# Performance work log

Measured on AMD Instinct MI355X. Metric: run time of the kernel, lower is better.

Reference implementation:

```python
import jax, jax.numpy as jnp
import numpy as np

NUM_CAPSULE = 16
DIM_CAPSULE = 32
ROUTINGS = 4
EPS = 1e-07


def squash(x, axis=-1):
    # NOTE: faithful to the source: x / sqrt(sum(x^2) + eps) (unit-norm style),
    # NOT the standard Hinton squash.
    s2 = jnp.sum(x * x, axis=axis, keepdims=True)
    return x / jnp.sqrt(s2 + EPS)


def setup_inputs() -> dict:
    key = jax.random.key(0)
    k1, k2 = jax.random.split(key)
    B, N_in, D_in = 128, 1024, 256
    x = jax.random.normal(k1, (B, N_in, D_in), dtype=jnp.float32)
    # xavier_normal over (1, D_in, NUM_CAPSULE*DIM_CAPSULE)
    fan_in, fan_out = D_in, NUM_CAPSULE * DIM_CAPSULE
    std = np.sqrt(2.0 / (fan_in + fan_out))
    W = jax.random.normal(k2, (1, D_in, NUM_CAPSULE * DIM_CAPSULE), dtype=jnp.float32) * std
    return {"x": x, "W": W}


def reference(x, W):
    B, N_in, _ = x.shape
    # u_hat: [B, N_in, num_cap*dim_cap] -> [B, num_cap, N_in, dim_cap]
    u_hat = jnp.matmul(x, W[0])
    u_hat = u_hat.reshape(B, N_in, NUM_CAPSULE, DIM_CAPSULE).transpose(0, 2, 1, 3)

    b = jnp.zeros((B, NUM_CAPSULE, N_in), dtype=u_hat.dtype)
    outputs = None
    for i in range(ROUTINGS):
        # torch permutes to softmax over the num_capsule axis; equivalent to axis=1 here
        c = jax.nn.softmax(b, axis=1)                      # [B, num_cap, N_in]
        outputs = squash(jnp.einsum('bij,bijk->bik', c, u_hat))  # [B, num_cap, dim_cap]
        if i < ROUTINGS - 1:
            b = jnp.einsum('bik,bijk->bij', outputs, u_hat)
    return outputs
```

## Files before the change

kernel.cpp:

```cpp
#include <hip/hip_runtime.h>

typedef unsigned int u32;
typedef unsigned short u16;
typedef float f32x4 __attribute__((ext_vector_type(4)));
typedef __bf16 bf16x8 __attribute__((ext_vector_type(8)));

#define BATCH 128
#define NIN   1024
#define DIN   256
#define NC    16
#define DC    32
#define NCOL  512

__device__ __forceinline__ float bflo(u32 v){ return __uint_as_float(v << 16); }
__device__ __forceinline__ float bfhi(u32 v){ return __uint_as_float(v & 0xffff0000u); }
__device__ __forceinline__ u32 bfround(u32 ua){ return (ua + 0x7fffu + ((ua >> 16) & 1u)) >> 16; }
__device__ __forceinline__ u32 pack2(float a, float b){
    return (bfround(__float_as_uint(a)) & 0xffffu) | (bfround(__float_as_uint(b)) << 16);
}
__device__ __forceinline__ bf16x8 ldfrag(const u16* p){
    return __builtin_bit_cast(bf16x8, *(const uint4*)p);
}

__device__ __forceinline__ int lds_x(int r, int d){
    int sw = (d >> 2) ^ ((r & 7) << 1) ^ (((r >> 3) & 3) << 2);
    return r * 256 + (sw << 2) + (d & 3);
}

__global__ __launch_bounds__(256) void k_pre(const float* __restrict__ x, const float* __restrict__ W,
                                             uint4* __restrict__ xbT, u16* __restrict__ xb,
                                             float* __restrict__ s, uint2* __restrict__ Wb,
                                             uint2* __restrict__ WT){
    __shared__ __align__(16) u16 xt[64 * 256];
    const int t = threadIdx.x, jc8 = blockIdx.x, b = blockIdx.y;

    if (jc8 == 0){
        int id = b * 256 + t;
        float4 w4 = ((const float4*)W)[id];
        Wb[id] = make_uint2(pack2(w4.x, w4.y), pack2(w4.z, w4.w));
        int c = id >> 6, d4 = id & 63;
        float e0 = W[(size_t)(d4 * 4 + 0) * NCOL + c];
        float e1 = W[(size_t)(d4 * 4 + 1) * NCOL + c];
        float e2 = W[(size_t)(d4 * 4 + 2) * NCOL + c];
        float e3 = W[(size_t)(d4 * 4 + 3) * NCOL + c];
        WT[c * 64 + d4] = make_uint2(pack2(e0, e1), pack2(e2, e3));
    }
    {
        const float4* xg = (const float4*)(x + ((size_t)b * NIN + jc8 * 64) * DIN);
        uint2* xbw = (uint2*)xb + ((size_t)(b * NIN + jc8 * 64)) * 64;
        int d4 = t & 63;
        #pragma unroll
        for (int m = 0; m < 16; m++){
            int r = (t >> 6) + 4 * m;
            float4 v = xg[r * 64 + d4];
            uint2 p = make_uint2(pack2(v.x, v.y), pack2(v.z, v.w));
            *(uint2*)&xt[lds_x(r, d4 * 4)] = p;
            xbw[r * 64 + d4] = p;
        }
    }
    __syncthreads();
    {
        float acc = 0.f;
        #pragma unroll
        for (int r = 0; r < 64; r++) acc += bflo((u32)xt[lds_x(r, t)]);
        atomicAdd(&s[b * DIN + t], acc);
    }
    #pragma unroll
    for (int w = 0; w < 8; w++){
        int oid = t + 256 * w;
        int lane = oid & 63, js2 = (oid >> 6) & 1, dt = oid >> 7;
        int l15 = lane & 15, q = lane >> 4;
        int rb = js2 * 32 + q * 8, d = dt * 16 + l15;
        u32 r[4];
        #pragma unroll
        for (int p = 0; p < 4; p++){
            u32 lo = xt[lds_x(rb + 2 * p, d)];
            u32 hi = xt[lds_x(rb + 2 * p + 1, d)];
            r[p] = lo | (hi << 16);
        }
        xbT[(((size_t)b * 16 + dt) * 32 + (jc8 * 2 + js2)) * 64 + lane] = make_uint4(r[0], r[1], r[2], r[3]);
    }
}

__global__ __launch_bounds__(256) void k_main(const u16* __restrict__ xb, const uint4* __restrict__ xbT,
                                              const u16* __restrict__ vb, float* __restrict__ zp){
    __shared__ float bbl[16][132];
    __shared__ __align__(16) u16 cl[16][136];
    const int t = threadIdx.x, jh = blockIdx.x, b = blockIdx.y;
    const int lane = t & 63, wv = t >> 6;
    const int l15 = lane & 15, q = lane >> 4;

    uint4 vfrag[8];
    #pragma unroll
    for (int ks = 0; ks < 8; ks++)
        vfrag[ks] = *(const uint4*)&vb[((size_t)b * 16 + l15) * 256 + ks * 32 + q * 8];

    const u16* xrow = xb + ((size_t)(b * NIN + jh * 128)) * 256;
    #pragma unroll
    for (int u = 0; u < 2; u++){
        int jt = wv * 2 + u;
        const u16* xr = xrow + (jt * 16 + l15) * 256 + q * 8;
        f32x4 acc = {0.f, 0.f, 0.f, 0.f};
        #pragma unroll
        for (int ks = 0; ks < 8; ks++)
            acc = __builtin_amdgcn_mfma_f32_16x16x32_bf16(
                __builtin_bit_cast(bf16x8, vfrag[ks]), ldfrag(xr + ks * 32), acc, 0, 0, 0);
        #pragma unroll
        for (int r = 0; r < 4; r++) bbl[q * 4 + r][jt * 16 + l15] = acc[r];
    }
    __syncthreads();

    if (t < 128){
        float mx = -1e30f, e[16], sum = 0.f;
        #pragma unroll
        for (int i = 0; i < 16; i++) mx = fmaxf(mx, bbl[i][t]);
        #pragma unroll
        for (int i = 0; i < 16; i++){ e[i] = __expf(bbl[i][t] - mx); sum += e[i]; }
        float inv = 1.f / sum;
        #pragma unroll
        for (int i = 0; i < 16; i++) cl[i][t] = (u16)bfround(__float_as_uint(e[i] * inv));
    }
    __syncthreads();

    bf16x8 cfrag[4];
    #pragma unroll
    for (int ksj = 0; ksj < 4; ksj++)
        cfrag[ksj] = __builtin_bit_cast(bf16x8, *(const uint4*)&cl[l15][ksj * 32 + q * 8]);
    #pragma unroll
    for (int u = 0; u < 4; u++){
        int dt = wv * 4 + u;
        f32x4 acc = {0.f, 0.f, 0.f, 0.f};
        #pragma unroll
        for (int ksj = 0; ksj < 4; ksj++){
            uint4 bw = xbT[(((size_t)b * 16 + dt) * 32 + jh * 4 + ksj) * 64 + lane];
            acc = __builtin_amdgcn_mfma_f32_16x16x32_bf16(
                cfrag[ksj], __builtin_bit_cast(bf16x8, bw), acc, 0, 0, 0);
        }
        float* zpb = zp + ((((size_t)jh * 128 + b) * 16) * 256) + dt * 16 + l15;
        #pragma unroll
        for (int r = 0; r < 4; r++) zpb[(size_t)(q * 4 + r) * 256] = acc[r];
    }
}

__global__ __launch_bounds__(256) void k_tail(const float* __restrict__ s, const float* __restrict__ zp,
                                              const u16* __restrict__ Wb, const u32* __restrict__ WT32,
                                              u16* __restrict__ vb, float* __restrict__ out, int mode){
    __shared__ float zl[8][260];
    __shared__ __align__(16) float ol[256];
    const int ih2 = blockIdx.x, b = blockIdx.y, t = threadIdx.x;
    const int i_loc = t >> 5;
    const int o_idx = ih2 * 256 + t;
    float y = 0.f;
    if (mode == 0){
        zl[0][t] = s[b * 256 + t] * (1.f / 16.f);
        __syncthreads();
        #pragma unroll 8
        for (int d = 0; d < 256; d++) y += zl[0][d] * bflo((u32)Wb[d * 512 + o_idx]);
    } else {
        #pragma unroll
        for (int u0 = 0; u0 < 8; u0++){
            int idx = t + 256 * u0;
            int ii = idx >> 8, dd = idx & 255;
            int ig = ih2 * 8 + ii;
            float acc = 0.f;
            #pragma unroll
            for (int jh = 0; jh < 8; jh++)
                acc += zp[((((size_t)jh * 128 + b) * 16 + ig) * 256) + dd];
            zl[ii][dd] = acc;
        }
        __syncthreads();
        #pragma unroll 8
        for (int d = 0; d < 256; d++) y += zl[i_loc][d] * bflo((u32)Wb[d * 512 + o_idx]);
    }
    float s2 = y * y;
    s2 += __shfl_xor(s2, 1); s2 += __shfl_xor(s2, 2); s2 += __shfl_xor(s2, 4);
    s2 += __shfl_xor(s2, 8); s2 += __shfl_xor(s2, 16);
    float r = y / sqrtf(s2 + 1e-7f);
    if (mode == 2){ out[b * 512 + o_idx] = r; return; }
    ol[t] = r;
    __syncthreads();
    {
        int dh = t & 127, ihalf = t >> 7;
        #pragma unroll
        for (int e = 0; e < 4; e++){
            int ii = ihalf * 4 + e;
            int i2 = ih2 * 8 + ii;
            float a0 = 0.f, a1 = 0.f;
            #pragma unroll
            for (int k = 0; k < 32; k++){
                u32 wv2 = WT32[(size_t)(i2 * 32 + k) * 128 + dh];
                float ok = ol[ii * 32 + k];
                a0 += ok * bflo(wv2); a1 += ok * bfhi(wv2);
            }
            ((u32*)vb)[(size_t)(b * 16 + i2) * 128 + dh] = pack2(a0, a1);
        }
    }
}

extern "C" void kernel_launch(void* const* d_in, const int* in_sizes, int n_in,
                              void* d_out, int out_size, void* d_ws, size_t ws_size,
                              hipStream_t stream){
    const float* x = (const float*)d_in[0];
    const float* W = (const float*)d_in[1];
    float* out = (float*)d_out;
    char* ws = (char*)d_ws;
    float* s    = (float*)(ws);
    u16*   vb   = (u16*)  (ws + 131072);
    u16*   Wb   = (u16*)  (ws + 1179648);
    u32*   WT   = (u32*)  (ws + 1441792);
    float* zp   = (float*)(ws + 1703936);
    u16*   xb   = (u16*)  (ws + 18481152);
    uint4* xbT  = (uint4*)(ws + 85590016);

    hipMemsetAsync(s, 0, 131072, stream);
    k_pre<<<dim3(16, BATCH), 256, 0, stream>>>(x, W, xbT, xb, s, (uint2*)Wb, (uint2*)WT);
    k_tail<<<dim3(2, BATCH), 256, 0, stream>>>(s, zp, Wb, WT, vb, out, 0);
    for (int it = 1; it < 4; it++){
        k_main<<<dim3(8, BATCH), 256, 0, stream>>>(xb, xbT, vb, zp);
        k_tail<<<dim3(2, BATCH), 256, 0, stream>>>(s, zp, Wb, WT, vb, out, it == 3 ? 2 : 1);
    }
}
```

Measured before the change: 361.9 us.

## Fuse routing iterations into one per-batch kernel and shrink preprocessing tiles

Replaces the seven alternating k_main/k_tail launches with a single k_fused kernel that runs one 1024-thread block per batch. That block does all routing iterations in shared memory, so the zp partial-sum round trips through global memory and the extra launches go away. k_pre now uses 32-row tiles and computes column sums in registers during conversion instead of in a second LDS pass. The trade-off is that only 128 blocks run, which lowers parallelism, and the fused block uses a lot of shared memory, which limits occupancy.

```diff
diff --git a/kernel.cpp b/kernel.cpp
--- a/kernel.cpp
+++ b/kernel.cpp
@@ -31,10 +31,10 @@
                                              uint4* __restrict__ xbT, u16* __restrict__ xb,
                                              float* __restrict__ s, uint2* __restrict__ Wb,
                                              uint2* __restrict__ WT){
-    __shared__ __align__(16) u16 xt[64 * 256];
-    const int t = threadIdx.x, jc8 = blockIdx.x, b = blockIdx.y;
-
-    if (jc8 == 0){
+    __shared__ __align__(16) u16 xt[32 * 256];
+    const int t = threadIdx.x, jc = blockIdx.x, b = blockIdx.y;
+
+    if (jc == 0){
         int id = b * 256 + t;
         float4 w4 = ((const float4*)W)[id];
         Wb[id] = make_uint2(pack2(w4.x, w4.y), pack2(w4.z, w4.w));
@@ -46,31 +46,32 @@
         WT[c * 64 + d4] = make_uint2(pack2(e0, e1), pack2(e2, e3));
     }
     {
-        const float4* xg = (const float4*)(x + ((size_t)b * NIN + jc8 * 64) * DIN);
-        uint2* xbw = (uint2*)xb + ((size_t)(b * NIN + jc8 * 64)) * 64;
-        int d4 = t & 63;
+        const float4* xg = (const float4*)(x + ((size_t)b * NIN + jc * 32) * DIN);
+        uint2* xbw = (uint2*)xb + ((size_t)(b * NIN + jc * 32)) * 64;
+        int d4 = t & 63, rg = t >> 6;
+        float cs0 = 0.f, cs1 = 0.f, cs2 = 0.f, cs3 = 0.f;
         #pragma unroll
-        for (int m = 0; m < 16; m++){
-            int r = (t >> 6) + 4 * m;
+        for (int m = 0; m < 8; m++){
+            int r = rg + 4 * m;
             float4 v = xg[r * 64 + d4];
             uint2 p = make_uint2(pack2(v.x, v.y), pack2(v.z, v.w));
             *(uint2*)&xt[lds_x(r, d4 * 4)] = p;
             xbw[r * 64 + d4] = p;
-        }
+            cs0 += bflo(p.x); cs1 += bfhi(p.x);
+            cs2 += bflo(p.y); cs3 += bfhi(p.y);
+        }
+        atomicAdd(&s[b * DIN + d4 * 4 + 0], cs0);
+        atomicAdd(&s[b * DIN + d4 * 4 + 1], cs1);
+        atomicAdd(&s[b * DIN + d4 * 4 + 2], cs2);
+        atomicAdd(&s[b * DIN + d4 * 4 + 3], cs3);
     }
     __syncthreads();
-    {
-        float acc = 0.f;
-        #pragma unroll
-        for (int r = 0; r < 64; r++) acc += bflo((u32)xt[lds_x(r, t)]);
-        atomicAdd(&s[b * DIN + t], acc);
-    }
     #pragma unroll
-    for (int w = 0; w < 8; w++){
+    for (int w = 0; w < 4; w++){
         int oid = t + 256 * w;
-        int lane = oid & 63, js2 = (oid >> 6) & 1, dt = oid >> 7;
+        int lane = oid & 63, dt = oid >> 6;
         int l15 = lane & 15, q = lane >> 4;
-        int rb = js2 * 32 + q * 8, d = dt * 16 + l15;
+        int rb = q * 8, d = dt * 16 + l15;
         u32 r[4];
         #pragma unroll
         for (int p = 0; p < 4; p++){
@@ -78,121 +79,118 @@
             u32 hi = xt[lds_x(rb + 2 * p + 1, d)];
             r[p] = lo | (hi << 16);
         }
-        xbT[(((size_t)b * 16 + dt) * 32 + (jc8 * 2 + js2)) * 64 + lane] = make_uint4(r[0], r[1], r[2], r[3]);
-    }
-}
-
-__global__ __launch_bounds__(256) void k_main(const u16* __restrict__ xb, const uint4* __restrict__ xbT,
-                                              const u16* __restrict__ vb, float* __restrict__ zp){
-    __shared__ float bbl[16][132];
-    __shared__ __align__(16) u16 cl[16][136];
-    const int t = threadIdx.x, jh = blockIdx.x, b = blockIdx.y;
+        xbT[(((size_t)b * 16 + dt) * 32 + jc) * 64 + lane] = make_uint4(r[0], r[1], r[2], r[3]);
+    }
+}
+
+__global__ __launch_bounds__(1024) void k_fused(const u16* __restrict__ xb, const uint4* __restrict__ xbT,
+                                                const float* __restrict__ s, const u16* __restrict__ Wb,
+                                                const u32* __restrict__ WT32, float* __restrict__ out){
+    __shared__ float bbl[16 * 1028];
+    __shared__ __align__(16) u16 cl[16 * 1032];
+    __shared__ float zl[16 * 260];
+    __shared__ __align__(16) float ol[512];
+    __shared__ __align__(16) u32 vfb[8 * 256];
+    __shared__ float yp[1024];
+    const int b = blockIdx.x, t = threadIdx.x;
     const int lane = t & 63, wv = t >> 6;
     const int l15 = lane & 15, q = lane >> 4;
 
-    uint4 vfrag[8];
-    #pragma unroll
-    for (int ks = 0; ks < 8; ks++)
-        vfrag[ks] = *(const uint4*)&vb[((size_t)b * 16 + l15) * 256 + ks * 32 + q * 8];
-
-    const u16* xrow = xb + ((size_t)(b * NIN + jh * 128)) * 256;
-    #pragma unroll
-    for (int u = 0; u < 2; u++){
-        int jt = wv * 2 + u;
-        const u16* xr = xrow + (jt * 16 + l15) * 256 + q * 8;
-        f32x4 acc = {0.f, 0.f, 0.f, 0.f};
-        #pragma unroll
-        for (int ks = 0; ks < 8; ks++)
-            acc = __builtin_amdgcn_mfma_f32_16x16x32_bf16(
-                __builtin_bit_cast(bf16x8, vfrag[ks]), ldfrag(xr + ks * 32), acc, 0, 0, 0);
-        #pragma unroll
-        for (int r = 0; r < 4; r++) bbl[q * 4 + r][jt * 16 + l15] = acc[r];
-    }
-    __syncthreads();
-
-    if (t < 128){
-        float mx = -1e30f, e[16], sum = 0.f;
-        #pragma unroll
-        for (int i = 0; i < 16; i++) mx = fmaxf(mx, bbl[i][t]);
-        #pragma unroll
-        for (int i = 0; i < 16; i++){ e[i] = __expf(bbl[i][t] - mx); sum += e[i]; }
-        float inv = 1.f / sum;
-        #pragma unroll
-        for (int i = 0; i < 16; i++) cl[i][t] = (u16)bfround(__float_as_uint(e[i] * inv));
-    }
-    __syncthreads();
-
-    bf16x8 cfrag[4];
-    #pragma unroll
-    for (int ksj = 0; ksj < 4; ksj++)
-        cfrag[ksj] = __builtin_bit_cast(bf16x8, *(const uint4*)&cl[l15][ksj * 32 + q * 8]);
-    #pragma unroll
-    for (int u = 0; u < 4; u++){
-        int dt = wv * 4 + u;
-        f32x4 acc = {0.f, 0.f, 0.f, 0.f};
-        #pragma unroll
-        for (int ksj = 0; ksj < 4; ksj++){
-            uint4 bw = xbT[(((size_t)b * 16 + dt) * 32 + jh * 4 + ksj) * 64 + lane];
-            acc = __builtin_amdgcn_mfma_f32_16x16x32_bf16(
-                cfrag[ksj], __builtin_bit_cast(bf16x8, bw), acc, 0, 0, 0);
-        }
-        float* zpb = zp + ((((size_t)jh * 128 + b) * 16) * 256) + dt * 16 + l15;
-        #pragma unroll
-        for (int r = 0; r < 4; r++) zpb[(size_t)(q * 4 + r) * 256] = acc[r];
-    }
-}
-
-__global__ __launch_bounds__(256) void k_tail(const float* __restrict__ s, const float* __restrict__ zp,
-                                              const u16* __restrict__ Wb, const u32* __restrict__ WT32,
-                                              u16* __restrict__ vb, float* __restrict__ out, int mode){
-    __shared__ float zl[8][260];
-    __shared__ __align__(16) float ol[256];
-    const int ih2 = blockIdx.x, b = blockIdx.y, t = threadIdx.x;
-    const int i_loc = t >> 5;
-    const int o_idx = ih2 * 256 + t;
-    float y = 0.f;
-    if (mode == 0){
-        zl[0][t] = s[b * 256 + t] * (1.f / 16.f);
-        __syncthreads();
-        #pragma unroll 8
-        for (int d = 0; d < 256; d++) y += zl[0][d] * bflo((u32)Wb[d * 512 + o_idx]);
-    } else {
-        #pragma unroll
-        for (int u0 = 0; u0 < 8; u0++){
-            int idx = t + 256 * u0;
-            int ii = idx >> 8, dd = idx & 255;
-            int ig = ih2 * 8 + ii;
-            float acc = 0.f;
-            #pragma unroll
-            for (int jh = 0; jh < 8; jh++)
-                acc += zp[((((size_t)jh * 128 + b) * 16 + ig) * 256) + dd];
-            zl[ii][dd] = acc;
-        }
-        __syncthreads();
-        #pragma unroll 8
-        for (int d = 0; d < 256; d++) y += zl[i_loc][d] * bflo((u32)Wb[d * 512 + o_idx]);
-    }
-    float s2 = y * y;
-    s2 += __shfl_xor(s2, 1); s2 += __shfl_xor(s2, 2); s2 += __shfl_xor(s2, 4);
-    s2 += __shfl_xor(s2, 8); s2 += __shfl_xor(s2, 16);
-    float r = y / sqrtf(s2 + 1e-7f);
-    if (mode == 2){ out[b * 512 + o_idx] = r; return; }
-    ol[t] = r;
+    if (t < 256) zl[t] = s[b * 256 + t] * (1.f / 16.f);
     __syncthreads();
     {
-        int dh = t & 127, ihalf = t >> 7;
+        int h = t >> 9, c = t & 511;
+        const u16* wp = Wb + (size_t)(h * 128) * 512 + c;
+        float acc = 0.f;
+        #pragma unroll 8
+        for (int d = 0; d < 128; d++) acc += zl[h * 128 + d] * bflo((u32)wp[d * 512]);
+        yp[t] = acc;
+    }
+    __syncthreads();
+    if (t < 512){
+        float yv = yp[t] + yp[t + 512];
+        float s2 = yv * yv;
+        s2 += __shfl_xor(s2, 1); s2 += __shfl_xor(s2, 2); s2 += __shfl_xor(s2, 4);
+        s2 += __shfl_xor(s2, 8); s2 += __shfl_xor(s2, 16);
+        ol[t] = yv / sqrtf(s2 + 1e-7f);
+    }
+
+    for (int it = 1; it <= 3; ++it){
+        __syncthreads();
         #pragma unroll
-        for (int e = 0; e < 4; e++){
-            int ii = ihalf * 4 + e;
-            int i2 = ih2 * 8 + ii;
+        for (int e2 = 0; e2 < 2; e2++){
+            int wo = t + 1024 * e2;
+            int i = wo >> 7, dh = wo & 127;
             float a0 = 0.f, a1 = 0.f;
             #pragma unroll
             for (int k = 0; k < 32; k++){
-                u32 wv2 = WT32[(size_t)(i2 * 32 + k) * 128 + dh];
-                float ok = ol[ii * 32 + k];
+                u32 wv2 = WT32[(size_t)(i * 32 + k) * 128 + dh];
+                float ok = ol[i * 32 + k];
                 a0 += ok * bflo(wv2); a1 += ok * bfhi(wv2);
             }
-            ((u32*)vb)[(size_t)(b * 16 + i2) * 128 + dh] = pack2(a0, a1);
+            int ks = dh >> 4, qq = (dh >> 2) & 3, e = dh & 3;
+            vfb[ks * 256 + (qq * 16 + i) * 4 + e] = pack2(a0, a1);
+        }
+        __syncthreads();
+        {
+            uint4 vf[8];
+            #pragma unroll
+            for (int ks = 0; ks < 8; ks++) vf[ks] = *(const uint4*)&vfb[ks * 256 + lane * 4];
+            #pragma unroll
+            for (int u = 0; u < 4; u++){
+                int jt = wv * 4 + u;
+                const u16* xr = xb + ((size_t)(b * NIN + jt * 16 + l15)) * 256 + q * 8;
+                f32x4 acc = {0.f, 0.f, 0.f, 0.f};
+                #pragma unroll
+                for (int ks = 0; ks < 8; ks++)
+                    acc = __builtin_amdgcn_mfma_f32_16x16x32_bf16(
+                        __builtin_bit_cast(bf16x8, vf[ks]), ldfrag(xr + ks * 32), acc, 0, 0, 0);
+                #pragma unroll
+                for (int r = 0; r < 4; r++) bbl[(q * 4 + r) * 1028 + jt * 16 + l15] = acc[r];
+            }
+        }
+        __syncthreads();
+        {
+            float mx = -1e30f, e[16], sum = 0.f;
+            #pragma unroll
+            for (int i = 0; i < 16; i++) mx = fmaxf(mx, bbl[i * 1028 + t]);
+            #pragma unroll
+            for (int i = 0; i < 16; i++){ e[i] = __expf(bbl[i * 1028 + t] - mx); sum += e[i]; }
+            float inv = 1.f / sum;
+            #pragma unroll
+            for (int i = 0; i < 16; i++) cl[i * 1032 + t] = (u16)bfround(__float_as_uint(e[i] * inv));
+        }
+        __syncthreads();
+        {
+            int dt = wv;
+            f32x4 acc = {0.f, 0.f, 0.f, 0.f};
+            const uint4* xT = xbT + (((size_t)b * 16 + dt) * 32) * 64 + lane;
+            #pragma unroll 8
+            for (int js = 0; js < 32; js++){
+                bf16x8 cf = ldfrag(&cl[l15 * 1032 + js * 32 + q * 8]);
+                acc = __builtin_amdgcn_mfma_f32_16x16x32_bf16(cf, __builtin_bit_cast(bf16x8, xT[js * 64]), acc, 0, 0, 0);
+            }
+            #pragma unroll
+            for (int r = 0; r < 4; r++) zl[(q * 4 + r) * 260 + dt * 16 + l15] = acc[r];
+        }
+        __syncthreads();
+        {
+            int h = t >> 9, c = t & 511, i = c >> 5;
+            const u16* wp = Wb + (size_t)(h * 128) * 512 + c;
+            float acc = 0.f;
+            #pragma unroll 8
+            for (int d = 0; d < 128; d++) acc += zl[i * 260 + h * 128 + d] * bflo((u32)wp[d * 512]);
+            yp[t] = acc;
+        }
+        __syncthreads();
+        if (t < 512){
+            float yv = yp[t] + yp[t + 512];
+            float s2 = yv * yv;
+            s2 += __shfl_xor(s2, 1); s2 += __shfl_xor(s2, 2); s2 += __shfl_xor(s2, 4);
+            s2 += __shfl_xor(s2, 8); s2 += __shfl_xor(s2, 16);
+            float r = yv / sqrtf(s2 + 1e-7f);
+            if (it == 3) out[b * NCOL + t] = r;
+            else         ol[t] = r;
         }
     }
 }
@@ -205,18 +203,12 @@
     float* out = (float*)d_out;
     char* ws = (char*)d_ws;
     float* s    = (float*)(ws);
-    u16*   vb   = (u16*)  (ws + 131072);
-    u16*   Wb   = (u16*)  (ws + 1179648);
-    u32*   WT   = (u32*)  (ws + 1441792);
-    float* zp   = (float*)(ws + 1703936);
-    u16*   xb   = (u16*)  (ws + 18481152);
-    uint4* xbT  = (uint4*)(ws + 85590016);
+    u16*   Wb   = (u16*)  (ws + 131072);
+    u32*   WT   = (u32*)  (ws + 393216);
+    u16*   xb   = (u16*)  (ws + 655360);
+    uint4* xbT  = (uint4*)(ws + 67764224);
 
     hipMemsetAsync(s, 0, 131072, stream);
-    k_pre<<<dim3(16, BATCH), 256, 0, stream>>>(x, W, xbT, xb, s, (uint2*)Wb, (uint2*)WT);
-    k_tail<<<dim3(2, BATCH), 256, 0, stream>>>(s, zp, Wb, WT, vb, out, 0);
-    for (int it = 1; it < 4; it++){
-        k_main<<<dim3(8, BATCH), 256, 0, stream>>>(xb, xbT, vb, zp);
-        k_tail<<<dim3(2, BATCH), 256, 0, stream>>>(s, zp, Wb, WT, vb, out, it == 3 ? 2 : 1);
-    }
-}
+    k_pre<<<dim3(32, BATCH), 256, 0, stream>>>(x, W, xbT, xb, s, (uint2*)Wb, (uint2*)WT);
+    k_fused<<<BATCH, 1024, 0, stream>>>(xb, xbT, s, Wb, WT, out);
+}
```

Measured after the change: 544.9 us. 50.5% more time.

## Drop transposed bf16 copy of x; stage tile in LDS and atomically reduce z

Applied to the files above, without the earlier changes.

k_pre no longer writes a pre-transposed copy of x (xbT). It computes per-column sums in registers instead of going through LDS. k_main now loads its 128x256 bf16 tile of x into swizzled LDS once and reads it both row-wise and column-wise for the two MFMA passes, which halves the global traffic for x per routing iteration. The per-chunk partial z buffer is replaced by atomicAdd into a single accumulator that k_tail reads and clears, removing the 8-way partial reduction. The cost is 64KB of LDS per block, which lowers occupancy, plus strided LDS gathers and atomic contention.

```diff
diff --git a/kernel.cpp b/kernel.cpp
--- a/kernel.cpp
+++ b/kernel.cpp
@@ -28,13 +28,11 @@
 }
 
 __global__ __launch_bounds__(256) void k_pre(const float* __restrict__ x, const float* __restrict__ W,
-                                             uint4* __restrict__ xbT, u16* __restrict__ xb,
-                                             float* __restrict__ s, uint2* __restrict__ Wb,
-                                             uint2* __restrict__ WT){
-    __shared__ __align__(16) u16 xt[64 * 256];
-    const int t = threadIdx.x, jc8 = blockIdx.x, b = blockIdx.y;
-
-    if (jc8 == 0){
+                                             u16* __restrict__ xb, float* __restrict__ s,
+                                             uint2* __restrict__ Wb, uint2* __restrict__ WT){
+    const int t = threadIdx.x, seg = blockIdx.x, b = blockIdx.y;
+
+    if (seg == 0){
         int id = b * 256 + t;
         float4 w4 = ((const float4*)W)[id];
         Wb[id] = make_uint2(pack2(w4.x, w4.y), pack2(w4.z, w4.w));
@@ -45,66 +43,60 @@
         float e3 = W[(size_t)(d4 * 4 + 3) * NCOL + c];
         WT[c * 64 + d4] = make_uint2(pack2(e0, e1), pack2(e2, e3));
     }
-    {
-        const float4* xg = (const float4*)(x + ((size_t)b * NIN + jc8 * 64) * DIN);
-        uint2* xbw = (uint2*)xb + ((size_t)(b * NIN + jc8 * 64)) * 64;
-        int d4 = t & 63;
-        #pragma unroll
-        for (int m = 0; m < 16; m++){
-            int r = (t >> 6) + 4 * m;
-            float4 v = xg[r * 64 + d4];
-            uint2 p = make_uint2(pack2(v.x, v.y), pack2(v.z, v.w));
-            *(uint2*)&xt[lds_x(r, d4 * 4)] = p;
-            xbw[r * 64 + d4] = p;
-        }
-    }
-    __syncthreads();
-    {
-        float acc = 0.f;
-        #pragma unroll
-        for (int r = 0; r < 64; r++) acc += bflo((u32)xt[lds_x(r, t)]);
-        atomicAdd(&s[b * DIN + t], acc);
-    }
-    #pragma unroll
-    for (int w = 0; w < 8; w++){
-        int oid = t + 256 * w;
-        int lane = oid & 63, js2 = (oid >> 6) & 1, dt = oid >> 7;
-        int l15 = lane & 15, q = lane >> 4;
-        int rb = js2 * 32 + q * 8, d = dt * 16 + l15;
-        u32 r[4];
-        #pragma unroll
-        for (int p = 0; p < 4; p++){
-            u32 lo = xt[lds_x(rb + 2 * p, d)];
-            u32 hi = xt[lds_x(rb + 2 * p + 1, d)];
-            r[p] = lo | (hi << 16);
-        }
-        xbT[(((size_t)b * 16 + dt) * 32 + (jc8 * 2 + js2)) * 64 + lane] = make_uint4(r[0], r[1], r[2], r[3]);
-    }
-}
-
-__global__ __launch_bounds__(256) void k_main(const u16* __restrict__ xb, const uint4* __restrict__ xbT,
-                                              const u16* __restrict__ vb, float* __restrict__ zp){
+    const float4* xg = (const float4*)(x + ((size_t)b * NIN + seg * 64) * DIN);
+    uint2* xbw = (uint2*)xb + ((size_t)(b * NIN + seg * 64)) * 64;
+    int d4 = t & 63, r0 = t >> 6;
+    float cs0 = 0.f, cs1 = 0.f, cs2 = 0.f, cs3 = 0.f;
+    #pragma unroll
+    for (int m = 0; m < 16; m++){
+        int r = r0 + 4 * m;
+        float4 v = xg[r * 64 + d4];
+        uint2 p = make_uint2(pack2(v.x, v.y), pack2(v.z, v.w));
+        xbw[r * 64 + d4] = p;
+        cs0 += bflo(p.x); cs1 += bfhi(p.x);
+        cs2 += bflo(p.y); cs3 += bfhi(p.y);
+    }
+    atomicAdd(&s[b * DIN + d4 * 4 + 0], cs0);
+    atomicAdd(&s[b * DIN + d4 * 4 + 1], cs1);
+    atomicAdd(&s[b * DIN + d4 * 4 + 2], cs2);
+    atomicAdd(&s[b * DIN + d4 * 4 + 3], cs3);
+}
+
+__global__ __launch_bounds__(256) void k_main(const u16* __restrict__ xb, const u16* __restrict__ vb,
+                                              float* __restrict__ zg){
+    __shared__ __align__(16) u16 xt[128 * 256];
     __shared__ float bbl[16][132];
     __shared__ __align__(16) u16 cl[16][136];
     const int t = threadIdx.x, jh = blockIdx.x, b = blockIdx.y;
     const int lane = t & 63, wv = t >> 6;
     const int l15 = lane & 15, q = lane >> 4;
 
-    uint4 vfrag[8];
+    uint4 vf[8];
     #pragma unroll
     for (int ks = 0; ks < 8; ks++)
-        vfrag[ks] = *(const uint4*)&vb[((size_t)b * 16 + l15) * 256 + ks * 32 + q * 8];
-
-    const u16* xrow = xb + ((size_t)(b * NIN + jh * 128)) * 256;
+        vf[ks] = *(const uint4*)&vb[((size_t)b * 16 + l15) * 256 + ks * 32 + q * 8];
+
+    {
+        const uint4* xg = (const uint4*)(xb + ((size_t)(b * NIN + jh * 128)) * 256);
+        #pragma unroll
+        for (int m = 0; m < 16; m++){
+            int id = t + 256 * m;
+            int row = id >> 5, c8 = id & 31;
+            uint4 v = xg[id];
+            *(uint4*)&xt[lds_x(row, c8 * 8)] = v;
+        }
+    }
+    __syncthreads();
+
     #pragma unroll
     for (int u = 0; u < 2; u++){
         int jt = wv * 2 + u;
-        const u16* xr = xrow + (jt * 16 + l15) * 256 + q * 8;
         f32x4 acc = {0.f, 0.f, 0.f, 0.f};
         #pragma unroll
         for (int ks = 0; ks < 8; ks++)
             acc = __builtin_amdgcn_mfma_f32_16x16x32_bf16(
-                __builtin_bit_cast(bf16x8, vfrag[ks]), ldfrag(xr + ks * 32), acc, 0, 0, 0);
+                __builtin_bit_cast(bf16x8, vf[ks]),
+                ldfrag(&xt[lds_x(jt * 16 + l15, ks * 32 + q * 8)]), acc, 0, 0, 0);
         #pragma unroll
         for (int r = 0; r < 4; r++) bbl[q * 4 + r][jt * 16 + l15] = acc[r];
     }
@@ -122,27 +114,30 @@
     }
     __syncthreads();
 
-    bf16x8 cfrag[4];
-    #pragma unroll
-    for (int ksj = 0; ksj < 4; ksj++)
-        cfrag[ksj] = __builtin_bit_cast(bf16x8, *(const uint4*)&cl[l15][ksj * 32 + q * 8]);
     #pragma unroll
     for (int u = 0; u < 4; u++){
         int dt = wv * 4 + u;
         f32x4 acc = {0.f, 0.f, 0.f, 0.f};
         #pragma unroll
-        for (int ksj = 0; ksj < 4; ksj++){
-            uint4 bw = xbT[(((size_t)b * 16 + dt) * 32 + jh * 4 + ksj) * 64 + lane];
+        for (int js = 0; js < 4; js++){
+            u32 w[4];
+            #pragma unroll
+            for (int e2 = 0; e2 < 4; e2++){
+                u32 lo = xt[lds_x(js * 32 + q * 8 + 2 * e2,     dt * 16 + l15)];
+                u32 hi = xt[lds_x(js * 32 + q * 8 + 2 * e2 + 1, dt * 16 + l15)];
+                w[e2] = lo | (hi << 16);
+            }
+            bf16x8 cf = ldfrag(&cl[l15][js * 32 + q * 8]);
             acc = __builtin_amdgcn_mfma_f32_16x16x32_bf16(
-                cfrag[ksj], __builtin_bit_cast(bf16x8, bw), acc, 0, 0, 0);
-        }
-        float* zpb = zp + ((((size_t)jh * 128 + b) * 16) * 256) + dt * 16 + l15;
-        #pragma unroll
-        for (int r = 0; r < 4; r++) zpb[(size_t)(q * 4 + r) * 256] = acc[r];
-    }
-}
-
-__global__ __launch_bounds__(256) void k_tail(const float* __restrict__ s, const float* __restrict__ zp,
+                cf, __builtin_bit_cast(bf16x8, make_uint4(w[0], w[1], w[2], w[3])), acc, 0, 0, 0);
+        }
+        #pragma unroll
+        for (int r = 0; r < 4; r++)
+            atomicAdd(&zg[((size_t)b * 16 + q * 4 + r) * 256 + dt * 16 + l15], acc[r]);
+    }
+}
+
+__global__ __launch_bounds__(256) void k_tail(const float* __restrict__ s, float* __restrict__ zg,
                                               const u16* __restrict__ Wb, const u32* __restrict__ WT32,
                                               u16* __restrict__ vb, float* __restrict__ out, int mode){
     __shared__ float zl[8][260];
@@ -161,11 +156,9 @@
         for (int u0 = 0; u0 < 8; u0++){
             int idx = t + 256 * u0;
             int ii = idx >> 8, dd = idx & 255;
-            int ig = ih2 * 8 + ii;
-            float acc = 0.f;
-            #pragma unroll
-            for (int jh = 0; jh < 8; jh++)
-                acc += zp[((((size_t)jh * 128 + b) * 16 + ig) * 256) + dd];
+            size_t a = ((size_t)b * 16 + ih2 * 8 + ii) * 256 + dd;
+            float acc = zg[a];
+            if (mode == 1) zg[a] = 0.f;
             zl[ii][dd] = acc;
         }
         __syncthreads();
@@ -205,18 +198,17 @@
     float* out = (float*)d_out;
     char* ws = (char*)d_ws;
     float* s    = (float*)(ws);
-    u16*   vb   = (u16*)  (ws + 131072);
-    u16*   Wb   = (u16*)  (ws + 1179648);
-    u32*   WT   = (u32*)  (ws + 1441792);
-    float* zp   = (float*)(ws + 1703936);
-    u16*   xb   = (u16*)  (ws + 18481152);
-    uint4* xbT  = (uint4*)(ws + 85590016);
-
-    hipMemsetAsync(s, 0, 131072, stream);
-    k_pre<<<dim3(16, BATCH), 256, 0, stream>>>(x, W, xbT, xb, s, (uint2*)Wb, (uint2*)WT);
-    k_tail<<<dim3(2, BATCH), 256, 0, stream>>>(s, zp, Wb, WT, vb, out, 0);
+    float* zg   = (float*)(ws + 131072);
+    u16*   Wb   = (u16*)  (ws + 2228224);
+    u32*   WT   = (u32*)  (ws + 2490368);
+    u16*   vb   = (u16*)  (ws + 2752512);
+    u16*   xb   = (u16*)  (ws + 3801088);
+
+    hipMemsetAsync(ws, 0, 2228224, stream);
+    k_pre<<<dim3(16, BATCH), 256, 0, stream>>>(x, W, xb, s, (uint2*)Wb, (uint2*)WT);
+    k_tail<<<dim3(2, BATCH), 256, 0, stream>>>(s, zg, Wb, WT, vb, out, 0);
     for (int it = 1; it < 4; it++){
-        k_main<<<dim3(8, BATCH), 256, 0, stream>>>(xb, xbT, vb, zp);
-        k_tail<<<dim3(2, BATCH), 256, 0, stream>>>(s, zp, Wb, WT, vb, out, it == 3 ? 2 : 1);
-    }
-}
+        k_main<<<dim3(8, BATCH), 256, 0, stream>>>(xb, vb, zg);
+        k_tail<<<dim3(2, BATCH), 256, 0, stream>>>(s, zg, Wb, WT, vb, out, it == 3 ? 2 : 1);
+    }
+}
```

Result: faster. 341.7 us (-5.6%).
